# Kernel tuning notes

Hardware: AMD Instinct MI355X
Metric: run time of the kernel (lower is better)

Reference implementation:

```python
import jax, jax.numpy as jnp
import numpy as np

MARGIN = 1.0
NUM_CLASSES = 128


def setup_inputs() -> dict:
    key = jax.random.key(0)
    k1, k2, k3, k4, k5, k6 = jax.random.split(key, 6)
    B, D, C = 131072, 256, NUM_CLASSES
    return {
        "embeddings": jax.random.normal(k1, (B, D), dtype=jnp.float32),
        "labels": jax.random.randint(k2, (B,), 0, C),
        "W": jax.random.normal(k3, (C, D), dtype=jnp.float32),
        "b": jax.random.normal(k4, (C,), dtype=jnp.float32),
        "r_pos": jax.random.randint(k5, (B,), 0, 1000000007),
        "r_neg": jax.random.randint(k6, (B,), 0, 1000000007),
    }


def reference(embeddings, labels, W, b, r_pos, r_neg):
    B = embeddings.shape[0]
    C = W.shape[0]
    labels = labels.astype(jnp.int32)
    r_pos = r_pos.astype(jnp.int32)
    r_neg = r_neg.astype(jnp.int32)

    # ---- classifier under no_grad: argmax/top-2 of softmax == of logits ----
    logits = jax.lax.stop_gradient(embeddings) @ W.T + b  # [B, C]
    _, top2 = jax.lax.top_k(logits, 2)
    predicted = top2[:, 0]
    runner_up = top2[:, 1]
    correct = predicted == labels
    target_neg = jnp.where(correct, runner_up, predicted)  # [B]

    # ---- per-class segments: sort indices by label once ----
    counts = jnp.zeros((C,), jnp.int32).at[labels].add(1)      # [C]
    starts = jnp.cumsum(counts) - counts                       # [C] segment starts
    order = jnp.argsort(labels).astype(jnp.int32)              # [B] sorted-by-label index list
    inv = jnp.zeros((B,), jnp.int32).at[order].set(jnp.arange(B, dtype=jnp.int32))
    rank = inv - starts[labels]                                # anchor's position within its class segment

    # ---- vectorized masked random sampling ----
    n_pos = counts[labels] - 1                                 # positives exclude the anchor itself
    pr = r_pos % jnp.maximum(n_pos, 1)
    pr = pr + (pr >= rank).astype(jnp.int32)                   # skip over anchor's own slot
    pos_idx = order[starts[labels] + pr]

    n_neg = counts[target_neg]                                 # target_neg != label, anchor never in set
    nr = r_neg % jnp.maximum(n_neg, 1)
    neg_idx = order[starts[target_neg] + nr]

    # ---- triplet margin loss ----
    d_pos = jnp.linalg.norm(embeddings - embeddings[pos_idx], axis=1)
    d_neg = jnp.linalg.norm(embeddings - embeddings[neg_idx], axis=1)
    loss = jnp.maximum(d_pos - d_neg + MARGIN, 0.0)

    valid = (n_pos > 0) & (n_neg > 0)
    loss = loss * valid.astype(loss.dtype)
    denom = jnp.maximum(valid.sum(), 1).astype(loss.dtype)
    return loss.sum() / denom
```

## Files before the change

kernel.cpp:

```cpp
#include <hip/hip_runtime.h>
#include <cstdint>
#include <cstddef>

constexpr int D = 256;
constexpr int C = 128;
constexpr float MARGIN = 1.0f;

typedef __attribute__((ext_vector_type(8))) short short8;
typedef __attribute__((ext_vector_type(4))) float f32x4;

__device__ inline unsigned f2bf(float x) {
    unsigned u = __float_as_uint(x);
    return (u + 0x7FFFu + ((u >> 16) & 1u)) >> 16;
}

__device__ inline void cvt_split8(const float* xs, short8& h, short8& l) {
#pragma unroll
    for (int j = 0; j < 8; ++j) {
        float x = xs[j];
        unsigned hb = f2bf(x);
        h[j] = (short)hb;
        float hf = __uint_as_float(hb << 16);
        l[j] = (short)f2bf(x - hf);
    }
}

__device__ __forceinline__ void merge_top2(float& v1, int& i1, float& v2, int& i2,
                                           float w1, int j1, float w2, int j2)
{
    bool b = (w1 > v1) || (w1 == v1 && j1 < i1);
    float best_v = b ? w1 : v1; int best_i = b ? j1 : i1;
    float lose_v = b ? v1 : w1; int lose_i = b ? i1 : j1;
    float sec_v  = b ? w2 : v2; int sec_i  = b ? j2 : i2;
    bool c = (lose_v > sec_v) || (lose_v == sec_v && lose_i < sec_i);
    v1 = best_v; i1 = best_i;
    v2 = c ? lose_v : sec_v; i2 = c ? lose_i : sec_i;
}

__launch_bounds__(512, 4)
__global__ void k1_logits_top2(const float* __restrict__ emb,
                               const int*   __restrict__ labels,
                               const float* __restrict__ W,
                               const float* __restrict__ bias,
                               int*         __restrict__ target_neg,
                               unsigned short* __restrict__ embh,
                               int do_store)
{
    __shared__ char ldsW[C * 512];
    __shared__ float ldsBias[C];
    const int tid = threadIdx.x;

#pragma unroll
    for (int c = tid; c < 4096; c += 512) {
        int n = c >> 5, slot = c & 31;
        const float* src = W + n * 256 + slot * 8;
        float4 f0 = *(const float4*)src;
        float4 f1 = *(const float4*)(src + 4);
        short8 h;
        h[0] = (short)f2bf(f0.x); h[1] = (short)f2bf(f0.y);
        h[2] = (short)f2bf(f0.z); h[3] = (short)f2bf(f0.w);
        h[4] = (short)f2bf(f1.x); h[5] = (short)f2bf(f1.y);
        h[6] = (short)f2bf(f1.z); h[7] = (short)f2bf(f1.w);
        int dst = (n * 512 + slot * 16) ^ ((n & 7) << 4);
        *(short8*)(ldsW + dst) = h;
    }
    if (tid < C) ldsBias[tid] = bias[tid];
    __syncthreads();

    const int wid = tid >> 6, lane = tid & 63;
    const int l15 = lane & 15, lq = lane >> 4;
    const long row0 = (long)blockIdx.x * 256 + wid * 32;

    f32x4 acc[2][8];
#pragma unroll
    for (int rt = 0; rt < 2; ++rt)
#pragma unroll
        for (int t = 0; t < 8; ++t) acc[rt][t] = (f32x4){0.f, 0.f, 0.f, 0.f};

    const float* e0 = emb + (size_t)(row0 + l15) * D + 8 * lq;
    const float* e1 = e0 + (size_t)16 * D;
    char* eh0 = (char*)embh + (size_t)(row0 + l15) * 512 + 16 * lq;
    char* eh1 = eh0 + (size_t)16 * 512;
    const int xm = (l15 & 7) << 4;

    float4 pa0 = *(const float4*)(e0);
    float4 pa1 = *(const float4*)(e0 + 4);
    float4 pb0 = *(const float4*)(e1);
    float4 pb1 = *(const float4*)(e1 + 4);

#pragma unroll
    for (int s = 0; s < 8; ++s) {
        float x0[8], x1[8];
        *(float4*)&x0[0] = pa0; *(float4*)&x0[4] = pa1;
        *(float4*)&x1[0] = pb0; *(float4*)&x1[4] = pb1;
        if (s < 7) {
            pa0 = *(const float4*)(e0 + 32 * (s + 1));
            pa1 = *(const float4*)(e0 + 32 * (s + 1) + 4);
            pb0 = *(const float4*)(e1 + 32 * (s + 1));
            pb1 = *(const float4*)(e1 + 32 * (s + 1) + 4);
        }
        short8 a0h, a0l, a1h, a1l;
        cvt_split8(x0, a0h, a0l);
        cvt_split8(x1, a1h, a1l);
        if (do_store) {
            *(short8*)(eh0 + 64 * s) = a0h;
            *(short8*)(eh1 + 64 * s) = a1h;
        }
#pragma unroll
        for (int t = 0; t < 8; ++t) {
            int addr = ((16 * t + l15) * 512 + 64 * s + 16 * lq) ^ xm;
            short8 bh = *(const short8*)(ldsW + addr);
            acc[0][t] = __builtin_amdgcn_mfma_f32_16x16x32_bf16(a0h, bh, acc[0][t], 0, 0, 0);
            acc[0][t] = __builtin_amdgcn_mfma_f32_16x16x32_bf16(a0l, bh, acc[0][t], 0, 0, 0);
            acc[1][t] = __builtin_amdgcn_mfma_f32_16x16x32_bf16(a1h, bh, acc[1][t], 0, 0, 0);
            acc[1][t] = __builtin_amdgcn_mfma_f32_16x16x32_bf16(a1l, bh, acc[1][t], 0, 0, 0);
        }
    }

    float bv[8];
#pragma unroll
    for (int t = 0; t < 8; ++t) bv[t] = ldsBias[16 * t + l15];

    float v1[8], v2[8]; int i1[8], i2[8];
#pragma unroll
    for (int rt = 0; rt < 2; ++rt)
#pragma unroll
        for (int reg = 0; reg < 4; ++reg) {
            int sIdx = rt * 4 + reg;
            float a1 = -3.4e38f, a2 = -3.4e38f; int c1 = -1, c2 = -1;
#pragma unroll
            for (int t = 0; t < 8; ++t) {
                float v = acc[rt][t][reg] + bv[t];
                int c = 16 * t + l15;
                if (v > a1) { a2 = a1; c2 = c1; a1 = v; c1 = c; }
                else if (v > a2) { a2 = v; c2 = c; }
            }
            v1[sIdx] = a1; i1[sIdx] = c1; v2[sIdx] = a2; i2[sIdx] = c2;
        }
#pragma unroll
    for (int step = 1; step <= 8; step <<= 1) {
#pragma unroll
        for (int sIdx = 0; sIdx < 8; ++sIdx) {
            float w1 = __shfl_xor(v1[sIdx], step);
            int   j1 = __shfl_xor(i1[sIdx], step);
            float w2 = __shfl_xor(v2[sIdx], step);
            int   j2 = __shfl_xor(i2[sIdx], step);
            merge_top2(v1[sIdx], i1[sIdx], v2[sIdx], i2[sIdx], w1, j1, w2, j2);
        }
    }
    if (l15 == 0) {
#pragma unroll
        for (int rt = 0; rt < 2; ++rt)
#pragma unroll
            for (int reg = 0; reg < 4; ++reg) {
                int sIdx = rt * 4 + reg;
                long grow = row0 + rt * 16 + lq * 4 + reg;
                int lab = labels[grow];
                target_neg[grow] = (i1[sIdx] == lab) ? i2[sIdx] : i1[sIdx];
            }
    }
}

__global__ void k2_hist(const int* __restrict__ labels, int* __restrict__ hist)
{
    const int chunk = blockIdx.x * 4 + (threadIdx.x >> 6);
    const int lane = threadIdx.x & 63;
    const int lab = labels[chunk * 64 + lane];
    unsigned long long bal[7];
#pragma unroll
    for (int b = 0; b < 7; ++b) bal[b] = __ballot((lab >> b) & 1);
#pragma unroll
    for (int h = 0; h < 2; ++h) {
        const int c = lane + 64 * h;
        unsigned long long m = ~0ull;
#pragma unroll
        for (int b = 0; b < 7; ++b) m &= ((c >> b) & 1) ? bal[b] : ~bal[b];
        hist[chunk * C + c] = __popcll(m);
    }
}

__global__ void k3_scan(int* __restrict__ hist, int* __restrict__ counts, int nchunk)
{
    const int c = blockIdx.x;
    const int tid = threadIdx.x;
    const int per = nchunk / 256;
    int v[8];
    int s = 0;
#pragma unroll
    for (int j = 0; j < 8; ++j) {
        int x = (j < per) ? hist[(tid * per + j) * C + c] : 0;
        v[j] = s; s += x;
    }
    __shared__ int sm[256];
    sm[tid] = s;
    __syncthreads();
    for (int off = 1; off < 256; off <<= 1) {
        int x = (tid >= off) ? sm[tid - off] : 0;
        __syncthreads();
        sm[tid] += x;
        __syncthreads();
    }
    const int excl = sm[tid] - s;
#pragma unroll
    for (int j = 0; j < 8; ++j)
        if (j < per) hist[(tid * per + j) * C + c] = excl + v[j];
    if (tid == 255) counts[c] = sm[255];
}

__global__ void k3b_start(const int* __restrict__ counts, int* __restrict__ class_start)
{
    const int l = threadIdx.x;
    int c0 = counts[l], c1 = counts[l + 64];
    int x = c0, y = c1;
#pragma unroll
    for (int off = 1; off <= 32; off <<= 1) {
        int vx = __shfl_up(x, off);
        int vy = __shfl_up(y, off);
        if (l >= off) { x += vx; y += vy; }
    }
    int tot0 = __shfl(x, 63);
    class_start[l] = x - c0;
    class_start[64 + l] = tot0 + y - c1;
}

__global__ void k4_scatter(const int* __restrict__ labels, const int* __restrict__ hist,
                           const int* __restrict__ class_start,
                           int* __restrict__ order, int* __restrict__ rankArr)
{
    const int chunk = blockIdx.x * 4 + (threadIdx.x >> 6);
    const int lane = threadIdx.x & 63;
    const int i = chunk * 64 + lane;
    const int lab = labels[i];
    unsigned long long m = ~0ull;
#pragma unroll
    for (int b = 0; b < 7; ++b) {
        unsigned long long bal = __ballot((lab >> b) & 1);
        m &= ((lab >> b) & 1) ? bal : ~bal;
    }
    const int prefix = __popcll(m & ((1ull << lane) - 1ull));
    const int rank = hist[chunk * C + lab] + prefix;
    order[class_start[lab] + rank] = i;
    rankArr[i] = rank;
}

__global__ void k5a_sample(const int* __restrict__ labels, const int* __restrict__ target_neg,
                           const int* __restrict__ counts, const int* __restrict__ class_start,
                           const int* __restrict__ order, const int* __restrict__ rankArr,
                           const int* __restrict__ r_pos, const int* __restrict__ r_neg,
                           int* __restrict__ pos_idx, int* __restrict__ neg_idx, int B)
{
    const int i = blockIdx.x * blockDim.x + threadIdx.x;
    if (i >= B) return;
    const int lab = labels[i];
    const int tn = target_neg[i];
    const int n_pos = counts[lab] - 1;
    const int n_neg = counts[tn];
    int pr = r_pos[i] % max(n_pos, 1);
    pr += (pr >= rankArr[i]) ? 1 : 0;
    int ppos = class_start[lab] + pr; if (ppos > B - 1) ppos = B - 1;
    const int pidx = order[ppos];
    int nr = r_neg[i] % max(n_neg, 1);
    int npos = class_start[tn] + nr; if (npos > B - 1) npos = B - 1;
    const int nidx = order[npos];
    const bool valid = (n_pos > 0) && (n_neg > 0);
    pos_idx[i] = valid ? pidx : -1;
    neg_idx[i] = nidx;
}

__device__ inline void acc_pair(unsigned a, unsigned b, float& s) {
    float d0 = __uint_as_float(a << 16)         - __uint_as_float(b << 16);
    float d1 = __uint_as_float(a & 0xFFFF0000u) - __uint_as_float(b & 0xFFFF0000u);
    s = fmaf(d0, d0, s);
    s = fmaf(d1, d1, s);
}
__device__ inline void acc16(uint4 a, uint4 b, float& s) {
    acc_pair(a.x, b.x, s); acc_pair(a.y, b.y, s);
    acc_pair(a.z, b.z, s); acc_pair(a.w, b.w, s);
}

__launch_bounds__(256)
__global__ void k56_dist(const unsigned short* __restrict__ embh,
                         const float* __restrict__ embf,
                         const int* __restrict__ pos_idx, const int* __restrict__ neg_idx,
                         float* __restrict__ ploss, int* __restrict__ pcnt,
                         int B, int use_bf16)
{
    const int lane = threadIdx.x & 63;
    const int wid = threadIdx.x >> 6;
    const int l16 = threadIdx.x & 15;
    const int g = (blockIdx.x * blockDim.x + threadIdx.x) >> 4;
    const int ngroups = (gridDim.x * blockDim.x) >> 4;
    float lsum = 0.0f;
    int lcnt = 0;
    int p_next = (g < B) ? pos_idx[g] : -1;
    int n_next = (g < B) ? neg_idx[g] : 0;
    for (int row = g; row < B; row += ngroups) {
        const int p = p_next, n = n_next;
        const int nrow = row + ngroups;
        if (nrow < B) { p_next = pos_idx[nrow]; n_next = neg_idx[nrow]; }
        if (p >= 0) {
            float dp = 0.0f, dn = 0.0f;
            if (use_bf16) {
                const uint4* a4 = (const uint4*)(embh + (size_t)row * D);
                const uint4* p4 = (const uint4*)(embh + (size_t)p   * D);
                const uint4* n4 = (const uint4*)(embh + (size_t)n   * D);
                uint4 av0 = a4[2 * l16], av1 = a4[2 * l16 + 1];
                uint4 pv0 = p4[2 * l16], pv1 = p4[2 * l16 + 1];
                uint4 nv0 = n4[2 * l16], nv1 = n4[2 * l16 + 1];
                acc16(av0, pv0, dp); acc16(av1, pv1, dp);
                acc16(av0, nv0, dn); acc16(av1, nv1, dn);
            } else {
                const float4* a4 = (const float4*)(embf + (size_t)row * D);
                const float4* p4 = (const float4*)(embf + (size_t)p   * D);
                const float4* n4 = (const float4*)(embf + (size_t)n   * D);
#pragma unroll
                for (int j = 0; j < 4; ++j) {
                    float4 a  = a4[l16 + 16 * j];
                    float4 bp = p4[l16 + 16 * j];
                    float4 bn = n4[l16 + 16 * j];
                    float dx;
                    dx = a.x - bp.x; dp = fmaf(dx, dx, dp);
                    dx = a.y - bp.y; dp = fmaf(dx, dx, dp);
                    dx = a.z - bp.z; dp = fmaf(dx, dx, dp);
                    dx = a.w - bp.w; dp = fmaf(dx, dx, dp);
                    dx = a.x - bn.x; dn = fmaf(dx, dx, dn);
                    dx = a.y - bn.y; dn = fmaf(dx, dx, dn);
                    dx = a.z - bn.z; dn = fmaf(dx, dx, dn);
                    dx = a.w - bn.w; dn = fmaf(dx, dx, dn);
                }
            }
#pragma unroll
            for (int off = 8; off >= 1; off >>= 1) {
                dp += __shfl_xor(dp, off);
                dn += __shfl_xor(dn, off);
            }
            if (l16 == 0) {
                float l = sqrtf(dp) - sqrtf(dn) + MARGIN;
                lsum += fmaxf(l, 0.0f);
                lcnt += 1;
            }
        }
    }
    lsum += __shfl_xor(lsum, 16); lcnt += __shfl_xor(lcnt, 16);
    lsum += __shfl_xor(lsum, 32); lcnt += __shfl_xor(lcnt, 32);
    __shared__ float sl[4];
    __shared__ int   sc[4];
    if (lane == 0) { sl[wid] = lsum; sc[wid] = lcnt; }
    __syncthreads();
    if (threadIdx.x == 0) {
        ploss[blockIdx.x] = sl[0] + sl[1] + sl[2] + sl[3];
        pcnt[blockIdx.x]  = sc[0] + sc[1] + sc[2] + sc[3];
    }
}

__global__ void k6_final(const float* __restrict__ ploss, const int* __restrict__ pcnt,
                         float* __restrict__ out, int nb)
{
    const int tid = threadIdx.x;
    float s = 0.0f; int c = 0;
    for (int j = tid; j < nb; j += 256) { s += ploss[j]; c += pcnt[j]; }
    __shared__ float sf[256];
    __shared__ int   si[256];
    sf[tid] = s; si[tid] = c;
    __syncthreads();
    for (int off = 128; off >= 1; off >>= 1) {
        if (tid < off) { sf[tid] += sf[tid + off]; si[tid] += si[tid + off]; }
        __syncthreads();
    }
    if (tid == 0) out[0] = sf[0] / (float)max(si[0], 1);
}

extern "C" void kernel_launch(void* const* d_in, const int* in_sizes, int n_in,
                              void* d_out, int out_size, void* d_ws, size_t ws_size,
                              hipStream_t stream) {
    const float* emb    = (const float*)d_in[0];
    const int*   labels = (const int*)d_in[1];
    const float* W      = (const float*)d_in[2];
    const float* bias   = (const float*)d_in[3];
    const int*   r_pos  = (const int*)d_in[4];
    const int*   r_neg  = (const int*)d_in[5];
    float* out = (float*)d_out;

    const int B = in_sizes[1];
    const int nchunk = B / 64;
    const int NB5 = 2048;

    size_t off = 0;
    auto alloc = [&](size_t bytes) -> void* {
        void* p = (char*)d_ws + off;
        off += (bytes + 255) & ~(size_t)255;
        return p;
    };
    int* hist        = (int*)alloc((size_t)C * nchunk * 4);
    int* counts      = (int*)alloc(C * 4);
    int* class_start = (int*)alloc(C * 4);
    int* target_neg  = (int*)alloc((size_t)B * 4);
    int* rankArr     = (int*)alloc((size_t)B * 4);
    int* order       = (int*)alloc((size_t)B * 4);
    int* pos_idx     = (int*)alloc((size_t)B * 4);
    int* neg_idx     = (int*)alloc((size_t)B * 4);
    float* ploss     = (float*)alloc((size_t)NB5 * 4);
    int* pcnt        = (int*)alloc((size_t)NB5 * 4);
    if (off > ws_size) return;

    unsigned short* embh = (unsigned short*)alloc((size_t)B * D * 2);
    const int use_bf16 = (off <= ws_size) ? 1 : 0;

    k1_logits_top2<<<B / 256, 512, 0, stream>>>(emb, labels, W, bias, target_neg,
                                                use_bf16 ? embh : (unsigned short*)target_neg,
                                                use_bf16);
    k2_hist<<<nchunk / 4, 256, 0, stream>>>(labels, hist);
    k3_scan<<<C, 256, 0, stream>>>(hist, counts, nchunk);
    k3b_start<<<1, 64, 0, stream>>>(counts, class_start);
    k4_scatter<<<nchunk / 4, 256, 0, stream>>>(labels, hist, class_start, order, rankArr);
    k5a_sample<<<(B + 255) / 256, 256, 0, stream>>>(labels, target_neg, counts, class_start,
                                                    order, rankArr, r_pos, r_neg,
                                                    pos_idx, neg_idx, B);
    k56_dist<<<NB5, 256, 0, stream>>>(embh, emb, pos_idx, neg_idx, ploss, pcnt, B, use_bf16);
    k6_final<<<1, 256, 0, stream>>>(ploss, pcnt, out, NB5);
}
```

Measured before the change: 292.0 us.

## Precompute bf16 W, split classes across waves, and process two rows per dist iteration

```diff
diff --git a/kernel.cpp b/kernel.cpp
--- a/kernel.cpp
+++ b/kernel.cpp
@@ -37,127 +37,103 @@
     v2 = c ? lose_v : sec_v; i2 = c ? lose_i : sec_i;
 }
 
-__launch_bounds__(512, 4)
+__global__ void k0_convW(const float* __restrict__ W, unsigned short* __restrict__ Whi)
+{
+    int i = blockIdx.x * 256 + threadIdx.x;
+    Whi[i] = (unsigned short)f2bf(W[i]);
+}
+
+__launch_bounds__(256)
 __global__ void k1_logits_top2(const float* __restrict__ emb,
                                const int*   __restrict__ labels,
-                               const float* __restrict__ W,
+                               const unsigned short* __restrict__ Whi,
                                const float* __restrict__ bias,
                                int*         __restrict__ target_neg,
                                unsigned short* __restrict__ embh,
                                int do_store)
 {
-    __shared__ char ldsW[C * 512];
-    __shared__ float ldsBias[C];
+    __shared__ float4 shTop[2][2][16];
     const int tid = threadIdx.x;
-
-#pragma unroll
-    for (int c = tid; c < 4096; c += 512) {
-        int n = c >> 5, slot = c & 31;
-        const float* src = W + n * 256 + slot * 8;
-        float4 f0 = *(const float4*)src;
-        float4 f1 = *(const float4*)(src + 4);
-        short8 h;
-        h[0] = (short)f2bf(f0.x); h[1] = (short)f2bf(f0.y);
-        h[2] = (short)f2bf(f0.z); h[3] = (short)f2bf(f0.w);
-        h[4] = (short)f2bf(f1.x); h[5] = (short)f2bf(f1.y);
-        h[6] = (short)f2bf(f1.z); h[7] = (short)f2bf(f1.w);
-        int dst = (n * 512 + slot * 16) ^ ((n & 7) << 4);
-        *(short8*)(ldsW + dst) = h;
-    }
-    if (tid < C) ldsBias[tid] = bias[tid];
-    __syncthreads();
-
     const int wid = tid >> 6, lane = tid & 63;
+    const int rt = wid >> 1, ch = wid & 1;
     const int l15 = lane & 15, lq = lane >> 4;
-    const long row0 = (long)blockIdx.x * 256 + wid * 32;
-
-    f32x4 acc[2][8];
-#pragma unroll
-    for (int rt = 0; rt < 2; ++rt)
-#pragma unroll
-        for (int t = 0; t < 8; ++t) acc[rt][t] = (f32x4){0.f, 0.f, 0.f, 0.f};
+    const long row0 = (long)blockIdx.x * 32 + rt * 16;
+
+    f32x4 acc[4];
+#pragma unroll
+    for (int t = 0; t < 4; ++t) acc[t] = (f32x4){0.f, 0.f, 0.f, 0.f};
 
     const float* e0 = emb + (size_t)(row0 + l15) * D + 8 * lq;
-    const float* e1 = e0 + (size_t)16 * D;
     char* eh0 = (char*)embh + (size_t)(row0 + l15) * 512 + 16 * lq;
-    char* eh1 = eh0 + (size_t)16 * 512;
-    const int xm = (l15 & 7) << 4;
+    const char* wbase = (const char*)Whi + (ch * 64 + l15) * 512 + 16 * lq;
 
     float4 pa0 = *(const float4*)(e0);
     float4 pa1 = *(const float4*)(e0 + 4);
-    float4 pb0 = *(const float4*)(e1);
-    float4 pb1 = *(const float4*)(e1 + 4);
 
 #pragma unroll
     for (int s = 0; s < 8; ++s) {
-        float x0[8], x1[8];
+        float x0[8];
         *(float4*)&x0[0] = pa0; *(float4*)&x0[4] = pa1;
-        *(float4*)&x1[0] = pb0; *(float4*)&x1[4] = pb1;
         if (s < 7) {
             pa0 = *(const float4*)(e0 + 32 * (s + 1));
             pa1 = *(const float4*)(e0 + 32 * (s + 1) + 4);
-            pb0 = *(const float4*)(e1 + 32 * (s + 1));
-            pb1 = *(const float4*)(e1 + 32 * (s + 1) + 4);
-        }
-        short8 a0h, a0l, a1h, a1l;
-        cvt_split8(x0, a0h, a0l);
-        cvt_split8(x1, a1h, a1l);
-        if (do_store) {
-            *(short8*)(eh0 + 64 * s) = a0h;
-            *(short8*)(eh1 + 64 * s) = a1h;
-        }
-#pragma unroll
-        for (int t = 0; t < 8; ++t) {
-            int addr = ((16 * t + l15) * 512 + 64 * s + 16 * lq) ^ xm;
-            short8 bh = *(const short8*)(ldsW + addr);
-            acc[0][t] = __builtin_amdgcn_mfma_f32_16x16x32_bf16(a0h, bh, acc[0][t], 0, 0, 0);
-            acc[0][t] = __builtin_amdgcn_mfma_f32_16x16x32_bf16(a0l, bh, acc[0][t], 0, 0, 0);
-            acc[1][t] = __builtin_amdgcn_mfma_f32_16x16x32_bf16(a1h, bh, acc[1][t], 0, 0, 0);
-            acc[1][t] = __builtin_amdgcn_mfma_f32_16x16x32_bf16(a1l, bh, acc[1][t], 0, 0, 0);
-        }
-    }
-
-    float bv[8];
-#pragma unroll
-    for (int t = 0; t < 8; ++t) bv[t] = ldsBias[16 * t + l15];
-
-    float v1[8], v2[8]; int i1[8], i2[8];
-#pragma unroll
-    for (int rt = 0; rt < 2; ++rt)
-#pragma unroll
-        for (int reg = 0; reg < 4; ++reg) {
-            int sIdx = rt * 4 + reg;
-            float a1 = -3.4e38f, a2 = -3.4e38f; int c1 = -1, c2 = -1;
-#pragma unroll
-            for (int t = 0; t < 8; ++t) {
-                float v = acc[rt][t][reg] + bv[t];
-                int c = 16 * t + l15;
-                if (v > a1) { a2 = a1; c2 = c1; a1 = v; c1 = c; }
-                else if (v > a2) { a2 = v; c2 = c; }
-            }
-            v1[sIdx] = a1; i1[sIdx] = c1; v2[sIdx] = a2; i2[sIdx] = c2;
-        }
+        }
+        short8 ah, al;
+        cvt_split8(x0, ah, al);
+        if (do_store && ch == 0) *(short8*)(eh0 + 64 * s) = ah;
+#pragma unroll
+        for (int t = 0; t < 4; ++t) {
+            short8 bh = *(const short8*)(wbase + t * (16 * 512) + 64 * s);
+            acc[t] = __builtin_amdgcn_mfma_f32_16x16x32_bf16(ah, bh, acc[t], 0, 0, 0);
+            acc[t] = __builtin_amdgcn_mfma_f32_16x16x32_bf16(al, bh, acc[t], 0, 0, 0);
+        }
+    }
+
+    float bv[4];
+#pragma unroll
+    for (int t = 0; t < 4; ++t) bv[t] = bias[ch * 64 + 16 * t + l15];
+
+    float v1[4], v2[4]; int i1[4], i2[4];
+#pragma unroll
+    for (int reg = 0; reg < 4; ++reg) {
+        float a1 = -3.4e38f, a2 = -3.4e38f; int c1 = -1, c2 = -1;
+#pragma unroll
+        for (int t = 0; t < 4; ++t) {
+            float v = acc[t][reg] + bv[t];
+            int c = ch * 64 + 16 * t + l15;
+            if (v > a1) { a2 = a1; c2 = c1; a1 = v; c1 = c; }
+            else if (v > a2) { a2 = v; c2 = c; }
+        }
+        v1[reg] = a1; i1[reg] = c1; v2[reg] = a2; i2[reg] = c2;
+    }
 #pragma unroll
     for (int step = 1; step <= 8; step <<= 1) {
 #pragma unroll
-        for (int sIdx = 0; sIdx < 8; ++sIdx) {
-            float w1 = __shfl_xor(v1[sIdx], step);
-            int   j1 = __shfl_xor(i1[sIdx], step);
-            float w2 = __shfl_xor(v2[sIdx], step);
-            int   j2 = __shfl_xor(i2[sIdx], step);
-            merge_top2(v1[sIdx], i1[sIdx], v2[sIdx], i2[sIdx], w1, j1, w2, j2);
+        for (int r = 0; r < 4; ++r) {
+            float w1 = __shfl_xor(v1[r], step);
+            int   j1 = __shfl_xor(i1[r], step);
+            float w2 = __shfl_xor(v2[r], step);
+            int   j2 = __shfl_xor(i2[r], step);
+            merge_top2(v1[r], i1[r], v2[r], i2[r], w1, j1, w2, j2);
         }
     }
     if (l15 == 0) {
 #pragma unroll
-        for (int rt = 0; rt < 2; ++rt)
-#pragma unroll
-            for (int reg = 0; reg < 4; ++reg) {
-                int sIdx = rt * 4 + reg;
-                long grow = row0 + rt * 16 + lq * 4 + reg;
-                int lab = labels[grow];
-                target_neg[grow] = (i1[sIdx] == lab) ? i2[sIdx] : i1[sIdx];
-            }
+        for (int r = 0; r < 4; ++r)
+            shTop[rt][ch][lq * 4 + r] =
+                make_float4(v1[r], __int_as_float(i1[r]), v2[r], __int_as_float(i2[r]));
+    }
+    __syncthreads();
+    if (tid < 32) {
+        int rt2 = tid >> 4, rr = tid & 15;
+        float4 h0 = shTop[rt2][0][rr];
+        float4 h1 = shTop[rt2][1][rr];
+        float m1 = h0.x; int a1 = __float_as_int(h0.y);
+        float m2 = h0.z; int a2 = __float_as_int(h0.w);
+        merge_top2(m1, a1, m2, a2, h1.x, __float_as_int(h1.y), h1.z, __float_as_int(h1.w));
+        long grow = (long)blockIdx.x * 32 + tid;
+        int lab = labels[grow];
+        target_neg[grow] = (a1 == lab) ? a2 : a1;
     }
 }
 
@@ -292,53 +268,86 @@
     const int ngroups = (gridDim.x * blockDim.x) >> 4;
     float lsum = 0.0f;
     int lcnt = 0;
-    int p_next = (g < B) ? pos_idx[g] : -1;
-    int n_next = (g < B) ? neg_idx[g] : 0;
-    for (int row = g; row < B; row += ngroups) {
-        const int p = p_next, n = n_next;
-        const int nrow = row + ngroups;
-        if (nrow < B) { p_next = pos_idx[nrow]; n_next = neg_idx[nrow]; }
-        if (p >= 0) {
-            float dp = 0.0f, dn = 0.0f;
-            if (use_bf16) {
-                const uint4* a4 = (const uint4*)(embh + (size_t)row * D);
-                const uint4* p4 = (const uint4*)(embh + (size_t)p   * D);
-                const uint4* n4 = (const uint4*)(embh + (size_t)n   * D);
-                uint4 av0 = a4[2 * l16], av1 = a4[2 * l16 + 1];
-                uint4 pv0 = p4[2 * l16], pv1 = p4[2 * l16 + 1];
-                uint4 nv0 = n4[2 * l16], nv1 = n4[2 * l16 + 1];
-                acc16(av0, pv0, dp); acc16(av1, pv1, dp);
-                acc16(av0, nv0, dn); acc16(av1, nv1, dn);
-            } else {
-                const float4* a4 = (const float4*)(embf + (size_t)row * D);
-                const float4* p4 = (const float4*)(embf + (size_t)p   * D);
-                const float4* n4 = (const float4*)(embf + (size_t)n   * D);
+    for (int row = g * 2; row < B; row += ngroups * 2) {
+        const int r0 = row, r1 = row + 1;
+        const int p0 = pos_idx[r0], n0 = neg_idx[r0];
+        const bool has1 = (r1 < B);
+        const int p1 = has1 ? pos_idx[r1] : -1;
+        const int n1 = has1 ? neg_idx[r1] : 0;
+        float dp0 = 0.f, dn0 = 0.f, dp1 = 0.f, dn1 = 0.f;
+        if (use_bf16) {
+            uint4 a00, a01, pv00, pv01, nv00, nv01;
+            uint4 a10, a11, pv10, pv11, nv10, nv11;
+            if (p0 >= 0) {
+                const uint4* a4 = (const uint4*)(embh + (size_t)r0 * D);
+                const uint4* p4 = (const uint4*)(embh + (size_t)p0 * D);
+                const uint4* n4 = (const uint4*)(embh + (size_t)n0 * D);
+                a00 = a4[2 * l16]; a01 = a4[2 * l16 + 1];
+                pv00 = p4[2 * l16]; pv01 = p4[2 * l16 + 1];
+                nv00 = n4[2 * l16]; nv01 = n4[2 * l16 + 1];
+            }
+            if (p1 >= 0) {
+                const uint4* a4 = (const uint4*)(embh + (size_t)r1 * D);
+                const uint4* p4 = (const uint4*)(embh + (size_t)p1 * D);
+                const uint4* n4 = (const uint4*)(embh + (size_t)n1 * D);
+                a10 = a4[2 * l16]; a11 = a4[2 * l16 + 1];
+                pv10 = p4[2 * l16]; pv11 = p4[2 * l16 + 1];
+                nv10 = n4[2 * l16]; nv11 = n4[2 * l16 + 1];
+            }
+            if (p0 >= 0) {
+                acc16(a00, pv00, dp0); acc16(a01, pv01, dp0);
+                acc16(a00, nv00, dn0); acc16(a01, nv01, dn0);
+            }
+            if (p1 >= 0) {
+                acc16(a10, pv10, dp1); acc16(a11, pv11, dp1);
+                acc16(a10, nv10, dn1); acc16(a11, nv11, dn1);
+            }
+        } else {
+            if (p0 >= 0) {
+                const float4* a4 = (const float4*)(embf + (size_t)r0 * D);
+                const float4* p4 = (const float4*)(embf + (size_t)p0 * D);
+                const float4* n4 = (const float4*)(embf + (size_t)n0 * D);
 #pragma unroll
                 for (int j = 0; j < 4; ++j) {
-                    float4 a  = a4[l16 + 16 * j];
-                    float4 bp = p4[l16 + 16 * j];
-                    float4 bn = n4[l16 + 16 * j];
+                    float4 a = a4[l16 + 16 * j], bp = p4[l16 + 16 * j], bn = n4[l16 + 16 * j];
                     float dx;
-                    dx = a.x - bp.x; dp = fmaf(dx, dx, dp);
-                    dx = a.y - bp.y; dp = fmaf(dx, dx, dp);
-                    dx = a.z - bp.z; dp = fmaf(dx, dx, dp);
-                    dx = a.w - bp.w; dp = fmaf(dx, dx, dp);
-                    dx = a.x - bn.x; dn = fmaf(dx, dx, dn);
-                    dx = a.y - bn.y; dn = fmaf(dx, dx, dn);
-                    dx = a.z - bn.z; dn = fmaf(dx, dx, dn);
-                    dx = a.w - bn.w; dn = fmaf(dx, dx, dn);
+                    dx = a.x - bp.x; dp0 = fmaf(dx, dx, dp0);
+                    dx = a.y - bp.y; dp0 = fmaf(dx, dx, dp0);
+                    dx = a.z - bp.z; dp0 = fmaf(dx, dx, dp0);
+                    dx = a.w - bp.w; dp0 = fmaf(dx, dx, dp0);
+                    dx = a.x - bn.x; dn0 = fmaf(dx, dx, dn0);
+                    dx = a.y - bn.y; dn0 = fmaf(dx, dx, dn0);
+                    dx = a.z - bn.z; dn0 = fmaf(dx, dx, dn0);
+                    dx = a.w - bn.w; dn0 = fmaf(dx, dx, dn0);
                 }
             }
-#pragma unroll
-            for (int off = 8; off >= 1; off >>= 1) {
-                dp += __shfl_xor(dp, off);
-                dn += __shfl_xor(dn, off);
-            }
-            if (l16 == 0) {
-                float l = sqrtf(dp) - sqrtf(dn) + MARGIN;
-                lsum += fmaxf(l, 0.0f);
-                lcnt += 1;
-            }
+            if (p1 >= 0) {
+                const float4* a4 = (const float4*)(embf + (size_t)r1 * D);
+                const float4* p4 = (const float4*)(embf + (size_t)p1 * D);
+                const float4* n4 = (const float4*)(embf + (size_t)n1 * D);
+#pragma unroll
+                for (int j = 0; j < 4; ++j) {
+                    float4 a = a4[l16 + 16 * j], bp = p4[l16 + 16 * j], bn = n4[l16 + 16 * j];
+                    float dx;
+                    dx = a.x - bp.x; dp1 = fmaf(dx, dx, dp1);
+                    dx = a.y - bp.y; dp1 = fmaf(dx, dx, dp1);
+                    dx = a.z - bp.z; dp1 = fmaf(dx, dx, dp1);
+                    dx = a.w - bp.w; dp1 = fmaf(dx, dx, dp1);
+                    dx = a.x - bn.x; dn1 = fmaf(dx, dx, dn1);
+                    dx = a.y - bn.y; dn1 = fmaf(dx, dx, dn1);
+                    dx = a.z - bn.z; dn1 = fmaf(dx, dx, dn1);
+                    dx = a.w - bn.w; dn1 = fmaf(dx, dx, dn1);
+                }
+            }
+        }
+#pragma unroll
+        for (int off = 8; off >= 1; off >>= 1) {
+            dp0 += __shfl_xor(dp0, off); dn0 += __shfl_xor(dn0, off);
+            dp1 += __shfl_xor(dp1, off); dn1 += __shfl_xor(dn1, off);
+        }
+        if (l16 == 0) {
+            if (p0 >= 0) { lsum += fmaxf(sqrtf(dp0) - sqrtf(dn0) + MARGIN, 0.0f); lcnt += 1; }
+            if (p1 >= 0) { lsum += fmaxf(sqrtf(dp1) - sqrtf(dn1) + MARGIN, 0.0f); lcnt += 1; }
         }
     }
     lsum += __shfl_xor(lsum, 16); lcnt += __shfl_xor(lcnt, 16);
@@ -383,7 +392,7 @@
 
     const int B = in_sizes[1];
     const int nchunk = B / 64;
-    const int NB5 = 2048;
+    const int NB5 = 4096;
 
     size_t off = 0;
     auto alloc = [&](size_t bytes) -> void* {
@@ -401,14 +410,16 @@
     int* neg_idx     = (int*)alloc((size_t)B * 4);
     float* ploss     = (float*)alloc((size_t)NB5 * 4);
     int* pcnt        = (int*)alloc((size_t)NB5 * 4);
+    unsigned short* Whi = (unsigned short*)alloc((size_t)C * D * 2);
     if (off > ws_size) return;
 
     unsigned short* embh = (unsigned short*)alloc((size_t)B * D * 2);
     const int use_bf16 = (off <= ws_size) ? 1 : 0;
 
-    k1_logits_top2<<<B / 256, 512, 0, stream>>>(emb, labels, W, bias, target_neg,
-                                                use_bf16 ? embh : (unsigned short*)target_neg,
-                                                use_bf16);
+    k0_convW<<<(C * D) / 256, 256, 0, stream>>>(W, Whi);
+    k1_logits_top2<<<B / 32, 256, 0, stream>>>(emb, labels, Whi, bias, target_neg,
+                                               use_bf16 ? embh : (unsigned short*)target_neg,
+                                               use_bf16);
     k2_hist<<<nchunk / 4, 256, 0, stream>>>(labels, hist);
     k3_scan<<<C, 256, 0, stream>>>(hist, counts, nchunk);
     k3b_start<<<1, 64, 0, stream>>>(counts, class_start);
```

Result: slower. 330.6 us (+13.2%).

## Drop split-bf16 logits, pre-convert embeddings, batch four rows per group in distance kernel

Applied to the files above, without the earlier changes.

```diff
diff --git a/kernel.cpp b/kernel.cpp
--- a/kernel.cpp
+++ b/kernel.cpp
@@ -1,4 +1,5 @@
 #include <hip/hip_runtime.h>
+#include <hip/hip_bf16.h>
 #include <cstdint>
 #include <cstddef>
 
@@ -9,20 +10,10 @@
 typedef __attribute__((ext_vector_type(8))) short short8;
 typedef __attribute__((ext_vector_type(4))) float f32x4;
 
-__device__ inline unsigned f2bf(float x) {
-    unsigned u = __float_as_uint(x);
-    return (u + 0x7FFFu + ((u >> 16) & 1u)) >> 16;
-}
-
-__device__ inline void cvt_split8(const float* xs, short8& h, short8& l) {
-#pragma unroll
-    for (int j = 0; j < 8; ++j) {
-        float x = xs[j];
-        unsigned hb = f2bf(x);
-        h[j] = (short)hb;
-        float hf = __uint_as_float(hb << 16);
-        l[j] = (short)f2bf(x - hf);
-    }
+__device__ inline unsigned short f2bf16(float x) {
+    union { __hip_bfloat16 b; unsigned short u; } cv;
+    cv.b = __float2bfloat16(x);
+    return cv.u;
 }
 
 __device__ __forceinline__ void merge_top2(float& v1, int& i1, float& v2, int& i2,
@@ -37,14 +28,26 @@
     v2 = c ? lose_v : sec_v; i2 = c ? lose_i : sec_i;
 }
 
+__launch_bounds__(256)
+__global__ void kconv(const float* __restrict__ emb, unsigned short* __restrict__ embh)
+{
+    const size_t i = (size_t)blockIdx.x * 256 + threadIdx.x;
+    const float4* s = (const float4*)emb + 2 * i;
+    float4 f0 = s[0], f1 = s[1];
+    short8 h;
+    h[0] = (short)f2bf16(f0.x); h[1] = (short)f2bf16(f0.y);
+    h[2] = (short)f2bf16(f0.z); h[3] = (short)f2bf16(f0.w);
+    h[4] = (short)f2bf16(f1.x); h[5] = (short)f2bf16(f1.y);
+    h[6] = (short)f2bf16(f1.z); h[7] = (short)f2bf16(f1.w);
+    *((short8*)embh + i) = h;
+}
+
 __launch_bounds__(512, 4)
-__global__ void k1_logits_top2(const float* __restrict__ emb,
+__global__ void k1_logits_top2(const unsigned short* __restrict__ embh,
                                const int*   __restrict__ labels,
                                const float* __restrict__ W,
                                const float* __restrict__ bias,
-                               int*         __restrict__ target_neg,
-                               unsigned short* __restrict__ embh,
-                               int do_store)
+                               int*         __restrict__ target_neg)
 {
     __shared__ char ldsW[C * 512];
     __shared__ float ldsBias[C];
@@ -57,10 +60,10 @@
         float4 f0 = *(const float4*)src;
         float4 f1 = *(const float4*)(src + 4);
         short8 h;
-        h[0] = (short)f2bf(f0.x); h[1] = (short)f2bf(f0.y);
-        h[2] = (short)f2bf(f0.z); h[3] = (short)f2bf(f0.w);
-        h[4] = (short)f2bf(f1.x); h[5] = (short)f2bf(f1.y);
-        h[6] = (short)f2bf(f1.z); h[7] = (short)f2bf(f1.w);
+        h[0] = (short)f2bf16(f0.x); h[1] = (short)f2bf16(f0.y);
+        h[2] = (short)f2bf16(f0.z); h[3] = (short)f2bf16(f0.w);
+        h[4] = (short)f2bf16(f1.x); h[5] = (short)f2bf16(f1.y);
+        h[6] = (short)f2bf16(f1.z); h[7] = (short)f2bf16(f1.w);
         int dst = (n * 512 + slot * 16) ^ ((n & 7) << 4);
         *(short8*)(ldsW + dst) = h;
     }
@@ -77,43 +80,20 @@
 #pragma unroll
         for (int t = 0; t < 8; ++t) acc[rt][t] = (f32x4){0.f, 0.f, 0.f, 0.f};
 
-    const float* e0 = emb + (size_t)(row0 + l15) * D + 8 * lq;
-    const float* e1 = e0 + (size_t)16 * D;
-    char* eh0 = (char*)embh + (size_t)(row0 + l15) * 512 + 16 * lq;
-    char* eh1 = eh0 + (size_t)16 * 512;
+    const char* a0p = (const char*)embh + (size_t)(row0 + l15) * 512 + 16 * lq;
+    const char* a1p = a0p + (size_t)16 * 512;
     const int xm = (l15 & 7) << 4;
 
-    float4 pa0 = *(const float4*)(e0);
-    float4 pa1 = *(const float4*)(e0 + 4);
-    float4 pb0 = *(const float4*)(e1);
-    float4 pb1 = *(const float4*)(e1 + 4);
-
 #pragma unroll
     for (int s = 0; s < 8; ++s) {
-        float x0[8], x1[8];
-        *(float4*)&x0[0] = pa0; *(float4*)&x0[4] = pa1;
-        *(float4*)&x1[0] = pb0; *(float4*)&x1[4] = pb1;
-        if (s < 7) {
-            pa0 = *(const float4*)(e0 + 32 * (s + 1));
-            pa1 = *(const float4*)(e0 + 32 * (s + 1) + 4);
-            pb0 = *(const float4*)(e1 + 32 * (s + 1));
-            pb1 = *(const float4*)(e1 + 32 * (s + 1) + 4);
-        }
-        short8 a0h, a0l, a1h, a1l;
-        cvt_split8(x0, a0h, a0l);
-        cvt_split8(x1, a1h, a1l);
-        if (do_store) {
-            *(short8*)(eh0 + 64 * s) = a0h;
-            *(short8*)(eh1 + 64 * s) = a1h;
-        }
+        short8 ah0 = *(const short8*)(a0p + 64 * s);
+        short8 ah1 = *(const short8*)(a1p + 64 * s);
 #pragma unroll
         for (int t = 0; t < 8; ++t) {
             int addr = ((16 * t + l15) * 512 + 64 * s + 16 * lq) ^ xm;
             short8 bh = *(const short8*)(ldsW + addr);
-            acc[0][t] = __builtin_amdgcn_mfma_f32_16x16x32_bf16(a0h, bh, acc[0][t], 0, 0, 0);
-            acc[0][t] = __builtin_amdgcn_mfma_f32_16x16x32_bf16(a0l, bh, acc[0][t], 0, 0, 0);
-            acc[1][t] = __builtin_amdgcn_mfma_f32_16x16x32_bf16(a1h, bh, acc[1][t], 0, 0, 0);
-            acc[1][t] = __builtin_amdgcn_mfma_f32_16x16x32_bf16(a1l, bh, acc[1][t], 0, 0, 0);
+            acc[0][t] = __builtin_amdgcn_mfma_f32_16x16x32_bf16(ah0, bh, acc[0][t], 0, 0, 0);
+            acc[1][t] = __builtin_amdgcn_mfma_f32_16x16x32_bf16(ah1, bh, acc[1][t], 0, 0, 0);
         }
     }
 
@@ -280,66 +260,58 @@
 
 __launch_bounds__(256)
 __global__ void k56_dist(const unsigned short* __restrict__ embh,
-                         const float* __restrict__ embf,
                          const int* __restrict__ pos_idx, const int* __restrict__ neg_idx,
-                         float* __restrict__ ploss, int* __restrict__ pcnt,
-                         int B, int use_bf16)
+                         float* __restrict__ ploss, int* __restrict__ pcnt, int B)
 {
     const int lane = threadIdx.x & 63;
     const int wid = threadIdx.x >> 6;
     const int l16 = threadIdx.x & 15;
     const int g = (blockIdx.x * blockDim.x + threadIdx.x) >> 4;
-    const int ngroups = (gridDim.x * blockDim.x) >> 4;
     float lsum = 0.0f;
     int lcnt = 0;
-    int p_next = (g < B) ? pos_idx[g] : -1;
-    int n_next = (g < B) ? neg_idx[g] : 0;
-    for (int row = g; row < B; row += ngroups) {
-        const int p = p_next, n = n_next;
-        const int nrow = row + ngroups;
-        if (nrow < B) { p_next = pos_idx[nrow]; n_next = neg_idx[nrow]; }
-        if (p >= 0) {
-            float dp = 0.0f, dn = 0.0f;
-            if (use_bf16) {
-                const uint4* a4 = (const uint4*)(embh + (size_t)row * D);
-                const uint4* p4 = (const uint4*)(embh + (size_t)p   * D);
-                const uint4* n4 = (const uint4*)(embh + (size_t)n   * D);
-                uint4 av0 = a4[2 * l16], av1 = a4[2 * l16 + 1];
-                uint4 pv0 = p4[2 * l16], pv1 = p4[2 * l16 + 1];
-                uint4 nv0 = n4[2 * l16], nv1 = n4[2 * l16 + 1];
-                acc16(av0, pv0, dp); acc16(av1, pv1, dp);
-                acc16(av0, nv0, dn); acc16(av1, nv1, dn);
-            } else {
-                const float4* a4 = (const float4*)(embf + (size_t)row * D);
-                const float4* p4 = (const float4*)(embf + (size_t)p   * D);
-                const float4* n4 = (const float4*)(embf + (size_t)n   * D);
-#pragma unroll
-                for (int j = 0; j < 4; ++j) {
-                    float4 a  = a4[l16 + 16 * j];
-                    float4 bp = p4[l16 + 16 * j];
-                    float4 bn = n4[l16 + 16 * j];
-                    float dx;
-                    dx = a.x - bp.x; dp = fmaf(dx, dx, dp);
-                    dx = a.y - bp.y; dp = fmaf(dx, dx, dp);
-                    dx = a.z - bp.z; dp = fmaf(dx, dx, dp);
-                    dx = a.w - bp.w; dp = fmaf(dx, dx, dp);
-                    dx = a.x - bn.x; dn = fmaf(dx, dx, dn);
-                    dx = a.y - bn.y; dn = fmaf(dx, dx, dn);
-                    dx = a.z - bn.z; dn = fmaf(dx, dx, dn);
-                    dx = a.w - bn.w; dn = fmaf(dx, dx, dn);
-                }
-            }
-#pragma unroll
-            for (int off = 8; off >= 1; off >>= 1) {
-                dp += __shfl_xor(dp, off);
-                dn += __shfl_xor(dn, off);
-            }
-            if (l16 == 0) {
-                float l = sqrtf(dp) - sqrtf(dn) + MARGIN;
-                lsum += fmaxf(l, 0.0f);
+
+    int pI[4], nI[4];
+    uint4 av0[4], av1[4], pv0[4], pv1[4], nv0[4], nv1[4];
+#pragma unroll
+    for (int r = 0; r < 4; ++r) {
+        const int row = g * 4 + r;
+        pI[r] = pos_idx[row]; nI[r] = neg_idx[row];
+    }
+#pragma unroll
+    for (int r = 0; r < 4; ++r) {
+        const int row = g * 4 + r;
+        if (pI[r] >= 0) {
+            const uint4* a4 = (const uint4*)(embh + (size_t)row   * D);
+            const uint4* p4 = (const uint4*)(embh + (size_t)pI[r] * D);
+            const uint4* n4 = (const uint4*)(embh + (size_t)nI[r] * D);
+            av0[r] = a4[2 * l16]; av1[r] = a4[2 * l16 + 1];
+            pv0[r] = p4[2 * l16]; pv1[r] = p4[2 * l16 + 1];
+            nv0[r] = n4[2 * l16]; nv1[r] = n4[2 * l16 + 1];
+        }
+    }
+    float dp[4], dn[4];
+#pragma unroll
+    for (int r = 0; r < 4; ++r) {
+        dp[r] = 0.f; dn[r] = 0.f;
+        if (pI[r] >= 0) {
+            acc16(av0[r], pv0[r], dp[r]); acc16(av1[r], pv1[r], dp[r]);
+            acc16(av0[r], nv0[r], dn[r]); acc16(av1[r], nv1[r], dn[r]);
+        }
+    }
+#pragma unroll
+    for (int off = 8; off >= 1; off >>= 1)
+#pragma unroll
+        for (int r = 0; r < 4; ++r) {
+            dp[r] += __shfl_xor(dp[r], off);
+            dn[r] += __shfl_xor(dn[r], off);
+        }
+    if (l16 == 0) {
+#pragma unroll
+        for (int r = 0; r < 4; ++r)
+            if (pI[r] >= 0) {
+                lsum += fmaxf(sqrtf(dp[r]) - sqrtf(dn[r]) + MARGIN, 0.0f);
                 lcnt += 1;
             }
-        }
     }
     lsum += __shfl_xor(lsum, 16); lcnt += __shfl_xor(lcnt, 16);
     lsum += __shfl_xor(lsum, 32); lcnt += __shfl_xor(lcnt, 32);
@@ -401,14 +373,11 @@
     int* neg_idx     = (int*)alloc((size_t)B * 4);
     float* ploss     = (float*)alloc((size_t)NB5 * 4);
     int* pcnt        = (int*)alloc((size_t)NB5 * 4);
+    unsigned short* embh = (unsigned short*)alloc((size_t)B * D * 2);
     if (off > ws_size) return;
 
-    unsigned short* embh = (unsigned short*)alloc((size_t)B * D * 2);
-    const int use_bf16 = (off <= ws_size) ? 1 : 0;
-
-    k1_logits_top2<<<B / 256, 512, 0, stream>>>(emb, labels, W, bias, target_neg,
-                                                use_bf16 ? embh : (unsigned short*)target_neg,
-                                                use_bf16);
+    kconv<<<(B * (D / 8)) / 256, 256, 0, stream>>>(emb, embh);
+    k1_logits_top2<<<B / 256, 512, 0, stream>>>(embh, labels, W, bias, target_neg);
     k2_hist<<<nchunk / 4, 256, 0, stream>>>(labels, hist);
     k3_scan<<<C, 256, 0, stream>>>(hist, counts, nchunk);
     k3b_start<<<1, 64, 0, stream>>>(counts, class_start);
@@ -416,6 +385,6 @@
     k5a_sample<<<(B + 255) / 256, 256, 0, stream>>>(labels, target_neg, counts, class_start,
                                                     order, rankArr, r_pos, r_neg,
                                                     pos_idx, neg_idx, B);
-    k56_dist<<<NB5, 256, 0, stream>>>(embh, emb, pos_idx, neg_idx, ploss, pcnt, B, use_bf16);
+    k56_dist<<<NB5, 256, 0, stream>>>(embh, pos_idx, neg_idx, ploss, pcnt, B);
     k6_final<<<1, 256, 0, stream>>>(ploss, pcnt, out, NB5);
 }
```

After: 279.6 us. -4.2%, faster.
